# Performance work log

Measured on AMD Instinct MI355X. Metric: run time of the kernel, lower is better.

The kernel has to match this reference:

```python
import jax, jax.numpy as jnp
import numpy as np


def setup_inputs() -> dict:
    key = jax.random.key(0)
    k1, k2 = jax.random.split(key)
    B, M, N, D = 64, 16, 64, 1024
    src = jax.random.normal(k1, (B, N, D), dtype=jnp.float32)
    tgts = jax.random.normal(k2, (B, M, N, D), dtype=jnp.float32)
    return {"src": src, "tgts": tgts}


def reference(src, tgts):
    # loss = sum_{b,m,n} | dot(src[b,n], tgts[b,m,n]) |, returned as shape [1]
    dots = jnp.einsum("bnd,bmnd->bmn", src, tgts)  # [B, M, N]
    loss = jnp.sum(jnp.abs(dots))
    return loss.reshape(1)
```

## Files before the change

kernel.cpp:

```cpp
#include <hip/hip_runtime.h>


__global__ __launch_bounds__(256) void orth_loss_kernel(
    const float* __restrict__ src,
    const float* __restrict__ tgts,
    float* __restrict__ out,
    int total_rows)
{
    const int wave = threadIdx.x >> 6;
    const int lane = threadIdx.x & 63;

    float local = 0.0f;

    for (int row = blockIdx.x * 4 + wave; row < total_rows;
         row += gridDim.x * 4) {
        const int n  = row & 63;
        const int bm = row >> 6;
        const int b  = bm >> 4;

        const float4* __restrict__ tp =
            reinterpret_cast<const float4*>(tgts + (size_t)row * 1024);
        const float4* __restrict__ sp =
            reinterpret_cast<const float4*>(src + ((size_t)(b * 64 + n)) * 1024);

        float dot = 0.0f;
#pragma unroll
        for (int k = 0; k < 4; ++k) {
            const float4 t = tp[lane + k * 64];
            const float4 s = sp[lane + k * 64];
            dot = fmaf(t.x, s.x, dot);
            dot = fmaf(t.y, s.y, dot);
            dot = fmaf(t.z, s.z, dot);
            dot = fmaf(t.w, s.w, dot);
        }

#pragma unroll
        for (int off = 32; off > 0; off >>= 1)
            dot += __shfl_down(dot, off, 64);

        if (lane == 0) local += fabsf(dot);
    }

    __shared__ float sbuf[4];
    if (lane == 0) sbuf[wave] = local;
    __syncthreads();

    if (threadIdx.x == 0) {
        const float s = sbuf[0] + sbuf[1] + sbuf[2] + sbuf[3];
        atomicAdd(out, s);
    }
}

extern "C" void kernel_launch(void* const* d_in, const int* in_sizes, int n_in,
                              void* d_out, int out_size, void* d_ws, size_t ws_size,
                              hipStream_t stream) {
    const float* src  = (const float*)d_in[0];
    const float* tgts = (const float*)d_in[1];
    float* out = (float*)d_out;

    const int total_rows = in_sizes[1] / 1024;

    hipMemsetAsync(out, 0, sizeof(float), stream);

    const int blocks = 2048;
    orth_loss_kernel<<<blocks, 256, 0, stream>>>(src, tgts, out, total_rows);
}
```

Baseline: 57.20 us.

## Pipeline target rows through LDS ring with async global_load_lds and reuse src

Each wave now handles one (b, n) pair across eight m values. Target rows are streamed through a three-deep LDS ring using global_load_lds, with manual vmcnt waits so loads overlap compute, and the src row is loaded once and kept in registers. The memset and global atomic are replaced by per-block partials plus a second single-block reduction kernel. The aim is to cut src re-reads and expose more memory-level parallelism on this bandwidth-bound reduction, at the cost of an extra launch, fixed-shape assumptions and larger LDS use, which may lower occupancy.

```diff
diff --git a/kernel.cpp b/kernel.cpp
--- a/kernel.cpp
+++ b/kernel.cpp
@@ -1,54 +1,116 @@
 #include <hip/hip_runtime.h>
+#include <stdint.h>
 
 
-__global__ __launch_bounds__(256) void orth_loss_kernel(
+typedef __attribute__((ext_vector_type(4))) float f32x4;
+typedef const __attribute__((address_space(1))) void* gvp;
+typedef __attribute__((address_space(3))) void* svp;
+
+#define GLDS(gp, lp) \
+  __builtin_amdgcn_global_load_lds((gvp)(gp), (svp)(lp), 16, 0, 0)
+
+#define WAITV(n) asm volatile("s_waitcnt vmcnt(" #n ")" ::: "memory")
+#define CFENCE() asm volatile("" ::: "memory")
+
+__global__ __launch_bounds__(256) void orth_loss_main(
     const float* __restrict__ src,
     const float* __restrict__ tgts,
-    float* __restrict__ out,
-    int total_rows)
+    float* __restrict__ partials)
 {
+    __shared__ float ring[4][3][1024];
+    __shared__ float srcb[4][1024];
+    __shared__ float sbuf[4];
+
     const int wave = threadIdx.x >> 6;
     const int lane = threadIdx.x & 63;
 
-    float local = 0.0f;
+    const int w  = blockIdx.x * 4 + wave;
+    const int n  = w & 63;
+    const int t  = w >> 6;
+    const int mh = t & 1;
+    const int b  = t >> 1;
 
-    for (int row = blockIdx.x * 4 + wave; row < total_rows;
-         row += gridDim.x * 4) {
-        const int n  = row & 63;
-        const int bm = row >> 6;
-        const int b  = bm >> 4;
-
-        const float4* __restrict__ tp =
-            reinterpret_cast<const float4*>(tgts + (size_t)row * 1024);
-        const float4* __restrict__ sp =
-            reinterpret_cast<const float4*>(src + ((size_t)(b * 64 + n)) * 1024);
-
-        float dot = 0.0f;
-#pragma unroll
-        for (int k = 0; k < 4; ++k) {
-            const float4 t = tp[lane + k * 64];
-            const float4 s = sp[lane + k * 64];
-            dot = fmaf(t.x, s.x, dot);
-            dot = fmaf(t.y, s.y, dot);
-            dot = fmaf(t.z, s.z, dot);
-            dot = fmaf(t.w, s.w, dot);
-        }
+    const float* srow = src + ((size_t)(b * 64 + n)) * 1024 + lane * 4;
+    const int    base_row = (b * 16 + mh * 8) * 64 + n;
+    const float* trow = tgts + (size_t)base_row * 1024 + lane * 4;
+    const size_t mstride = (size_t)64 * 1024;
 
 #pragma unroll
-        for (int off = 32; off > 0; off >>= 1)
-            dot += __shfl_down(dot, off, 64);
-
-        if (lane == 0) local += fabsf(dot);
+    for (int k = 0; k < 4; ++k)
+        GLDS(srow + k * 256, &srcb[wave][k * 256]);
+#pragma unroll
+    for (int r = 0; r < 3; ++r) {
+#pragma unroll
+        for (int k = 0; k < 4; ++k)
+            GLDS(trow + r * mstride + k * 256, &ring[wave][r][k * 256]);
     }
 
-    __shared__ float sbuf[4];
+    float local = 0.0f;
+    f32x4 s0, s1, s2, s3;
+
+#define STEP(MI, DO_ISSUE, WN) do {                                          \
+      WAITV(WN);                                                             \
+      if ((MI) == 0) {                                                       \
+        const f32x4* sb_ = (const f32x4*)&srcb[wave][0];                     \
+        s0 = sb_[lane];       s1 = sb_[lane + 64];                           \
+        s2 = sb_[lane + 128]; s3 = sb_[lane + 192];                          \
+      }                                                                      \
+      const f32x4* lb_ = (const f32x4*)&ring[wave][(MI) % 3][0];             \
+      const f32x4 t0 = lb_[lane];                                            \
+      const f32x4 t1 = lb_[lane + 64];                                       \
+      const f32x4 t2 = lb_[lane + 128];                                      \
+      const f32x4 t3 = lb_[lane + 192];                                      \
+      float dot = 0.0f;                                                      \
+      dot = fmaf(t0.x, s0.x, dot); dot = fmaf(t0.y, s0.y, dot);              \
+      dot = fmaf(t0.z, s0.z, dot); dot = fmaf(t0.w, s0.w, dot);              \
+      dot = fmaf(t1.x, s1.x, dot); dot = fmaf(t1.y, s1.y, dot);              \
+      dot = fmaf(t1.z, s1.z, dot); dot = fmaf(t1.w, s1.w, dot);              \
+      dot = fmaf(t2.x, s2.x, dot); dot = fmaf(t2.y, s2.y, dot);              \
+      dot = fmaf(t2.z, s2.z, dot); dot = fmaf(t2.w, s2.w, dot);              \
+      dot = fmaf(t3.x, s3.x, dot); dot = fmaf(t3.y, s3.y, dot);              \
+      dot = fmaf(t3.z, s3.z, dot); dot = fmaf(t3.w, s3.w, dot);              \
+      _Pragma("unroll")                                                      \
+      for (int off = 32; off > 0; off >>= 1)                                 \
+          dot += __shfl_down(dot, off, 64);                                  \
+      if (lane == 0) local += fabsf(dot);                                    \
+      CFENCE();                    \
+      if (DO_ISSUE) {                                                        \
+        _Pragma("unroll")                                                    \
+        for (int k = 0; k < 4; ++k)                                          \
+            GLDS(trow + ((MI) + 3) * mstride + k * 256,                      \
+                 &ring[wave][(MI) % 3][k * 256]);                            \
+      }                                                                      \
+    } while (0)
+
+    STEP(0, 1, 8);
+    STEP(1, 1, 8);
+    STEP(2, 1, 8);
+    STEP(3, 1, 8);
+    STEP(4, 1, 8);
+    STEP(5, 0, 8);
+    STEP(6, 0, 4);
+    STEP(7, 0, 0);
+#undef STEP
+
     if (lane == 0) sbuf[wave] = local;
     __syncthreads();
+    if (threadIdx.x == 0)
+        partials[blockIdx.x] = sbuf[0] + sbuf[1] + sbuf[2] + sbuf[3];
+}
 
-    if (threadIdx.x == 0) {
-        const float s = sbuf[0] + sbuf[1] + sbuf[2] + sbuf[3];
-        atomicAdd(out, s);
-    }
+__global__ __launch_bounds__(256) void reduce_partials(
+    const float* __restrict__ partials, float* __restrict__ out, int n)
+{
+    __shared__ float sb[4];
+    const int lane = threadIdx.x & 63;
+    const int wv   = threadIdx.x >> 6;
+    float s = 0.0f;
+    for (int i = threadIdx.x; i < n; i += 256) s += partials[i];
+#pragma unroll
+    for (int off = 32; off > 0; off >>= 1) s += __shfl_down(s, off, 64);
+    if (lane == 0) sb[wv] = s;
+    __syncthreads();
+    if (threadIdx.x == 0) out[0] = sb[0] + sb[1] + sb[2] + sb[3];
 }
 
 extern "C" void kernel_launch(void* const* d_in, const int* in_sizes, int n_in,
@@ -56,12 +118,12 @@
                               hipStream_t stream) {
     const float* src  = (const float*)d_in[0];
     const float* tgts = (const float*)d_in[1];
-    float* out = (float*)d_out;
+    float* out      = (float*)d_out;
+    float* partials = (float*)d_ws;
 
-    const int total_rows = in_sizes[1] / 1024;
+    const int total_waves = (in_sizes[0] / 1024) * 2;
+    const int blocks = total_waves / 4;
 
-    hipMemsetAsync(out, 0, sizeof(float), stream);
-
-    const int blocks = 2048;
-    orth_loss_kernel<<<blocks, 256, 0, stream>>>(src, tgts, out, total_rows);
+    orth_loss_main<<<blocks, 256, 0, stream>>>(src, tgts, partials);
+    reduce_partials<<<1, 256, 0, stream>>>(partials, out, blocks);
 }
```

After: 50.28 us. 1.14x faster.
